# Kernel optimization log

Measured on AMD Instinct MI355X. Metric: run time of the kernel, lower is better.

Reference implementation:

```python
import jax, jax.numpy as jnp
import numpy as np

N = 50000          # n_sample
F = 64             # n_feature
DEG = 16           # edges per node
E = N * DEG
HID = 256          # n_hidden
NCLS = 16          # n_class
NPOOL = 3
K = 2              # propagation steps
ALPHA = 1.0        # Propagation alpha
EPS = 1e-5
NODE_POOL = round(N ** (1.0 / NPOOL))          # 37
N0 = round(N / NODE_POOL)                      # 1351
N1 = round(N0 / NODE_POOL)                     # 37
N2 = round(N1 / NODE_POOL)                     # 1


def setup_inputs():
    key = jax.random.key(0)
    ks = jax.random.split(key, 16)
    x = jax.random.normal(ks[0], (N, F), jnp.float32)
    x_cov = jax.random.uniform(ks[1], (N, F), jnp.float32)
    adj_rows = jnp.asarray(np.repeat(np.arange(N, dtype=np.int32), DEG))  # sorted
    adj_cols = jax.random.randint(ks[2], (E,), 0, N, jnp.int32)
    adj_vals = jax.random.uniform(ks[3], (E,), jnp.float32)
    feature_corr = jax.random.uniform(ks[4], (N2, F), jnp.float32)
    bn_gamma = jnp.ones((F,), jnp.float32)
    bn_beta = jnp.zeros((F,), jnp.float32)
    lin = lambda k, i, o: jax.random.normal(k, (i, o), jnp.float32) * 0.05
    W0 = lin(ks[5], F, HID); C0 = jax.random.normal(ks[6], (N0, HID), jnp.float32) * 0.05
    W1 = lin(ks[7], F, HID); C1 = jax.random.normal(ks[8], (N1, HID), jnp.float32) * 0.05
    W2 = lin(ks[9], F, HID); C2 = jax.random.normal(ks[10], (N2, HID), jnp.float32) * 0.05
    mW1 = lin(ks[11], 2 * F, HID); mb1 = jnp.zeros((HID,), jnp.float32)
    mp1 = jnp.full((1,), 0.25, jnp.float32)
    mW2 = lin(ks[12], HID, HID); mb2 = jnp.zeros((HID,), jnp.float32)
    mp2 = jnp.full((1,), 0.25, jnp.float32)
    mW3 = lin(ks[13], HID, NCLS); mb3 = jnp.zeros((NCLS,), jnp.float32)
    return dict(x=x, x_cov=x_cov, adj_vals=adj_vals, feature_corr=feature_corr,
                bn_gamma=bn_gamma, bn_beta=bn_beta, W0=W0, C0=C0, W1=W1, C1=C1,
                W2=W2, C2=C2, mW1=mW1, mb1=mb1, mp1=mp1, mW2=mW2, mb2=mb2, mp2=mp2,
                mW3=mW3, mb3=mb3, adj_rows=adj_rows, adj_cols=adj_cols)


def _pool(xc, W, C, nc):
    # ClusteringLayer: project, hard-assign to nearest centroid, mean-pool,
    # corr = per-node squared deviation from its cluster mean (input resolution).
    h = xc @ W                                                    # [n_prev, HID]
    d = (h * h).sum(-1, keepdims=True) - 2.0 * (h @ C.T) + (C * C).sum(-1)[None, :]
    a = jnp.argmin(d, axis=1)                                     # [n_prev] cluster ids
    cnt = jax.ops.segment_sum(jnp.ones((xc.shape[0],), xc.dtype), a, num_segments=nc)
    pooled = jax.ops.segment_sum(xc, a, num_segments=nc) / jnp.maximum(cnt, 1.0)[:, None]
    corr = (xc - pooled[a]) ** 2                                  # [n_prev, F]
    return pooled, corr, a


def _forward(x, x_cov, adj_vals, feature_corr, bn_gamma, bn_beta, W0, C0, W1, C1,
             W2, C2, mW1, mb1, mp1, mW2, mb2, mp2, mW3, mb3, adj_rows, adj_cols):
    # BatchNorm1d (batch statistics)
    mu = x.mean(0)
    var = x.var(0)
    x = (x - mu) / jnp.sqrt(var + EPS) * bn_gamma + bn_beta
    x0 = x
    # pooling hierarchy
    p0, corr0, a0 = _pool(x_cov, W0, C0, N0)
    p1, corr1, a1 = _pool(p0, W1, C1, N1)
    p2, corr2, a2 = _pool(p1, W2, C2, N2)
    loss = (corr1.mean(0) + corr2.mean(0)).mean() / (NPOOL - 1)
    # gains: spmm(hard assignment, corr_next) is a gather
    g0 = 2.0 * jax.nn.sigmoid(corr2[a1] - corr1)          # [N0, F]
    g1 = 2.0 * jax.nn.sigmoid(feature_corr[a2] - corr2)   # [N1, F]
    # composed node->level cluster ids (masks[1] = masks[0] @ masks[1])
    cl0 = a0               # [N]
    cl1 = a1[a0]           # [N]
    r, c = adj_rows, adj_cols
    # (M diag(g) M^T)[r,c] = g[cl(r)]^2 * 1[cl(r)==cl(c)], masked to adj pattern
    same0 = (cl0[r] == cl0[c])[:, None]
    same1 = (cl1[r] == cl1[c])[:, None]
    vals = adj_vals[:, None] \
        + jnp.where(same0, (g0 * g0)[cl0[r]], jnp.float32(0)) \
        + jnp.where(same1, (g1 * g1)[cl1[r]], jnp.float32(0))     # [E, F]
    # per-feature sparse row softmax
    m = jax.ops.segment_max(vals, r, num_segments=N)
    ev = jnp.exp(vals - m[r])
    s = jax.ops.segment_sum(ev, r, num_segments=N)
    A = ev / s[r]                                                  # [E, F]
    # k propagation steps: per-feature spmm + alpha * x0 residual
    for _ in range(K):
        x = jax.ops.segment_sum(A * x[c], r, num_segments=N) + ALPHA * x0
    # MLP head with PReLU, log-probabilities
    h = jnp.concatenate([x, x0], axis=1)
    h = h @ mW1 + mb1
    h = jnp.where(h >= 0, h, mp1 * h)
    h = h @ mW2 + mb2
    h = jnp.where(h >= 0, h, mp2 * h)
    logits = h @ mW3 + mb3
    out = jax.nn.log_softmax(logits, axis=1)
    return out, loss


def reference(x, x_cov, adj_vals, feature_corr, bn_gamma, bn_beta, W0, C0, W1, C1,
              W2, C2, mW1, mb1, mp1, mW2, mb2, mp2, mW3, mb3, adj_rows, adj_cols):
    return _forward(x, x_cov, adj_vals, feature_corr, bn_gamma, bn_beta, W0, C0,
                    W1, C1, W2, C2, mW1, mb1, mp1, mW2, mb2, mp2, mW3, mb3,
                    adj_rows, adj_cols)
```

## Files before the change

kernel.cpp:

```cpp
#include <hip/hip_runtime.h>
#include <math.h>

#define N_NODES 50000
#define FEA 64
#define DEG 16
#define HID 256
#define NCLS 16
#define NP0 1351
#define NP0T 1408
#define CTILES 11
#define NP1 37
#define EPSV 1e-5f

__global__ __launch_bounds__(256) void bn_reduce(const float* __restrict__ x,
                                                 float* __restrict__ bnsum, float* __restrict__ bnsq) {
    __shared__ float s1[256], s2[256];
    int tid = threadIdx.x;
    int f = tid & 63, sub = tid >> 6;
    float a = 0.f, b = 0.f;
    for (int r = blockIdx.x * 4 + sub; r < N_NODES; r += gridDim.x * 4) {
        float v = x[r * FEA + f];
        a += v; b += v * v;
    }
    s1[tid] = a; s2[tid] = b;
    __syncthreads();
    if (tid < 64) {
        a = s1[tid] + s1[tid + 64] + s1[tid + 128] + s1[tid + 192];
        b = s2[tid] + s2[tid + 64] + s2[tid + 128] + s2[tid + 192];
        atomicAdd(&bnsum[tid], a);
        atomicAdd(&bnsq[tid], b);
    }
}

__global__ __launch_bounds__(256) void bn_apply(const float* __restrict__ x,
                                                const float* __restrict__ bnsum, const float* __restrict__ bnsq,
                                                const float* __restrict__ gamma, const float* __restrict__ beta,
                                                float* __restrict__ x0) {
    int gid = blockIdx.x * 256 + threadIdx.x;
    if (gid >= N_NODES * FEA) return;
    int f = gid & 63;
    float mu = bnsum[f] * (1.0f / N_NODES);
    float var = bnsq[f] * (1.0f / N_NODES) - mu * mu;
    float sc = gamma[f] / sqrtf(var + EPSV);
    x0[gid] = (x[gid] - mu) * sc + beta[f];
}

__global__ void transpose_W0(const float* __restrict__ W0, float* __restrict__ W0t) {
    int idx = blockIdx.x * 256 + threadIdx.x;
    if (idx < FEA * HID) {
        int f = idx >> 8, h = idx & 255;
        W0t[h * FEA + f] = W0[idx];
    }
}

__global__ __launch_bounds__(64) void compute_G2(const float* __restrict__ W0t, const float* __restrict__ C0,
                                                 float* __restrict__ Gt, float* __restrict__ c0n) {
    int j = blockIdx.x, k = threadIdx.x;
    if (j >= NP0) {
        Gt[k * NP0T + j] = 0.f;
        if (k == 0) c0n[j] = 3.4e38f;
        return;
    }
    const float* c = C0 + j * HID;
    float acc = 0.f;
    for (int m = 0; m < HID; ++m) acc += W0t[m * FEA + k] * c[m];
    Gt[k * NP0T + j] = acc;
    float cn = 0.f;
    for (int m = k; m < HID; m += 64) { float v = c[m]; cn += v * v; }
    for (int off = 32; off; off >>= 1) cn += __shfl_xor(cn, off);
    if (k == 0) c0n[j] = cn;
}

__global__ void cnorm(const float* __restrict__ C, float* __restrict__ cn) {
    int j = blockIdx.x, k = threadIdx.x;
    const float* c = C + j * HID;
    float acc = 0.f;
    for (int m = k; m < HID; m += 64) { float v = c[m]; acc += v * v; }
    for (int off = 32; off; off >>= 1) acc += __shfl_xor(acc, off);
    if (k == 0) cn[j] = acc;
}

__global__ __launch_bounds__(256, 3) void argmin0_split(const float* __restrict__ xcov,
                                                        const float* __restrict__ Gt,
                                                        const float* __restrict__ c0n,
                                                        unsigned long long* __restrict__ amin) {
    __shared__ float As[64 * 140];
    __shared__ float Bs[32 * 128];
    __shared__ float cs[128];
    int t = threadIdx.x;
    int row0 = (blockIdx.x >> 2) * 128;
    int chunk = blockIdx.x & 3;
    int tile0 = chunk * 3;
    int tile1 = tile0 + 3; if (tile1 > CTILES) tile1 = CTILES;

    {
        int r = t & 127, half = t >> 7;
        int row = row0 + r;
        int fr = r + 4 * (r >> 5);
        if (row < N_NODES) {
            const float4* xp = (const float4*)(xcov + (size_t)row * FEA + half * 32);
            #pragma unroll
            for (int u = 0; u < 8; ++u) {
                float4 v = xp[u];
                int k = half * 32 + u * 4;
                As[(k+0)*140 + fr] = v.x; As[(k+1)*140 + fr] = v.y;
                As[(k+2)*140 + fr] = v.z; As[(k+3)*140 + fr] = v.w;
            }
        } else {
            #pragma unroll
            for (int u = 0; u < 8; ++u) {
                int k = half * 32 + u * 4;
                As[(k+0)*140+fr] = 0.f; As[(k+1)*140+fr] = 0.f;
                As[(k+2)*140+fr] = 0.f; As[(k+3)*140+fr] = 0.f;
            }
        }
    }

    int tr = t & 15, tc = t >> 4;
    int aoff = 8 * tr + 4 * (tr >> 2);
    int boff = 8 * tc;
    int bkk = t >> 3, bpart = t & 7;
    unsigned long long best[8];
    #pragma unroll
    for (int r = 0; r < 8; ++r) best[r] = ~0ull;

    for (int tile = tile0; tile < tile1; ++tile) {
        int j0 = tile * 128;
        float acc[8][8];
        #pragma unroll
        for (int r = 0; r < 8; ++r)
            #pragma unroll
            for (int c = 0; c < 8; ++c) acc[r][c] = 0.f;

        for (int kh = 0; kh < 2; ++kh) {
            __syncthreads();
            {
                const float* gr = Gt + (size_t)(kh * 32 + bkk) * NP0T + j0;
                #pragma unroll
                for (int u = 0; u < 4; ++u) {
                    int gi = bpart + 8 * u;
                    float4 v = *(const float4*)(gr + gi * 4);
                    *(float4*)(Bs + bkk * 128 + gi * 4) = v;
                }
            }
            if (kh == 0 && t < 128) cs[t] = c0n[j0 + t];
            __syncthreads();
            #pragma unroll 4
            for (int k2 = 0; k2 < 32; ++k2) {
                int k = kh * 32 + k2;
                float4 av0 = *(const float4*)(As + k * 140 + aoff);
                float4 av1 = *(const float4*)(As + k * 140 + aoff + 4);
                float4 bv0 = *(const float4*)(Bs + k2 * 128 + boff);
                float4 bv1 = *(const float4*)(Bs + k2 * 128 + boff + 4);
                float av[8] = {av0.x, av0.y, av0.z, av0.w, av1.x, av1.y, av1.z, av1.w};
                float bv[8] = {bv0.x, bv0.y, bv0.z, bv0.w, bv1.x, bv1.y, bv1.z, bv1.w};
                #pragma unroll
                for (int r = 0; r < 8; ++r)
                    #pragma unroll
                    for (int c = 0; c < 8; ++c) acc[r][c] += av[r] * bv[c];
            }
        }
        #pragma unroll
        for (int c = 0; c < 8; ++c) {
            int j = j0 + boff + c;
            float cn = cs[boff + c];
            #pragma unroll
            for (int r = 0; r < 8; ++r) {
                float d = cn - 2.0f * acc[r][c];
                unsigned s = __float_as_uint(d);
                unsigned u2 = ((int)s < 0) ? ~s : (s | 0x80000000u);
                unsigned long long p = ((unsigned long long)u2 << 32) | (unsigned)j;
                if (p < best[r]) best[r] = p;
            }
        }
    }

    __syncthreads();
    unsigned long long* pmin = (unsigned long long*)Bs;
    #pragma unroll
    for (int r = 0; r < 8; ++r) pmin[(8 * tr + r) * 16 + tc] = best[r];
    __syncthreads();
    if (t < 128) {
        unsigned long long b = pmin[t * 16];
        #pragma unroll
        for (int q = 1; q < 16; ++q) {
            unsigned long long v = pmin[t * 16 + q];
            if (v < b) b = v;
        }
        int row = row0 + t;
        if (row < N_NODES) atomicMin(&amin[row], b);
    }
}

__global__ __launch_bounds__(256) void hist0(const unsigned long long* __restrict__ amin,
                                             int* __restrict__ a0, int* __restrict__ hist) {
    int i = blockIdx.x * 256 + threadIdx.x;
    bool act = i < N_NODES;
    int j = act ? (int)(unsigned)amin[i] : -1;
    if (act) a0[i] = j;
    unsigned long long todo = __ballot(act);
    int lane = threadIdx.x & 63;
    while (todo) {
        int leader = __ffsll((long long)todo) - 1;
        int lj = __shfl(j, leader);
        unsigned long long grp = __ballot(act && j == lj);
        if (lane == leader) atomicAdd(&hist[lj], __popcll(grp));
        todo &= ~grp;
    }
}

__global__ __launch_bounds__(256) void scan0(const int* __restrict__ hist, int* __restrict__ off,
                                             int* __restrict__ cursor) {
    __shared__ int wsum[4];
    int t = threadIdx.x;
    int c0 = t * 6;
    int loc[6]; int s = 0;
    #pragma unroll
    for (int u = 0; u < 6; ++u) {
        int j = c0 + u;
        int h = (j < NP0) ? hist[j] : 0;
        loc[u] = s; s += h;
    }
    int lane = t & 63, w = t >> 6;
    int v = s;
    #pragma unroll
    for (int d = 1; d < 64; d <<= 1) {
        int up = __shfl_up(v, d);
        if (lane >= d) v += up;
    }
    if (lane == 63) wsum[w] = v;
    __syncthreads();
    int woff = 0;
    for (int q = 0; q < w; ++q) woff += wsum[q];
    int excl = woff + v - s;
    #pragma unroll
    for (int u = 0; u < 6; ++u) {
        int j = c0 + u;
        if (j < NP0) { off[j] = excl + loc[u]; cursor[j] = excl + loc[u]; }
    }
    if (t == 255) off[NP0] = excl + s;
}

__global__ __launch_bounds__(256) void scatter0(const int* __restrict__ a0, int* __restrict__ cursor,
                                                int* __restrict__ order, int* __restrict__ csrt) {
    int i = blockIdx.x * 256 + threadIdx.x;
    bool act = i < N_NODES;
    int j = act ? a0[i] : -1;
    int lane = threadIdx.x & 63;
    unsigned long long todo = __ballot(act);
    int pos = 0;
    while (todo) {
        int leader = __ffsll((long long)todo) - 1;
        int lj = __shfl(j, leader);
        unsigned long long grp = __ballot(act && j == lj);
        int base = 0;
        if (lane == leader) base = atomicAdd(&cursor[lj], __popcll(grp));
        base = __shfl(base, leader);
        if (act && j == lj)
            pos = base + __popcll(grp & ((1ull << lane) - 1ull));
        todo &= ~grp;
    }
    if (act) { order[pos] = i; csrt[pos] = j; }
}

__global__ __launch_bounds__(256) void pool0seg(const int* __restrict__ order, const int* __restrict__ csrt,
                                                const float* __restrict__ xcov, double* __restrict__ p0d) {
    int lane = threadIdx.x & 63;
    int w = threadIdx.x >> 6;
    int base = (blockIdx.x * 4 + w) * 16;
    if (base >= N_NODES) return;
    int n = N_NODES - base; if (n > 16) n = 16;
    float vals[16]; int cl[16];
    #pragma unroll
    for (int r = 0; r < 16; ++r) {
        if (r < n) {
            int idx = order[base + r];
            cl[r] = csrt[base + r];
            vals[r] = xcov[(size_t)idx * FEA + lane];
        } else { cl[r] = -1; vals[r] = 0.f; }
    }
    double acc = (double)vals[0]; int cur = cl[0];
    #pragma unroll
    for (int r = 1; r < 16; ++r) {
        if (r < n) {
            if (cl[r] == cur) { acc += (double)vals[r]; }
            else { atomicAdd(&p0d[(size_t)cur * FEA + lane], acc); acc = (double)vals[r]; cur = cl[r]; }
        }
    }
    atomicAdd(&p0d[(size_t)cur * FEA + lane], acc);
}

__global__ void pool_fin0(const double* __restrict__ p0d, const int* __restrict__ hist,
                          float* __restrict__ p0, int total) {
    int gid = blockIdx.x * 256 + threadIdx.x;
    if (gid < total) p0[gid] = (float)(p0d[gid] / (double)max(hist[gid >> 6], 1));
}

__global__ __launch_bounds__(64) void level1(const float* __restrict__ p0, const float* __restrict__ W1,
                                             const float* __restrict__ C1, const float* __restrict__ c1n,
                                             int* __restrict__ a1) {
    int i = blockIdx.x;
    int lane = threadIdx.x;
    const float* pr = p0 + (size_t)i * FEA;
    float h[4] = {0.f, 0.f, 0.f, 0.f};
    for (int k = 0; k < FEA; ++k) {
        float pv = pr[k];
        #pragma unroll
        for (int q = 0; q < 4; ++q) h[q] += pv * W1[k * HID + q * 64 + lane];
    }
    float hh = h[0]*h[0] + h[1]*h[1] + h[2]*h[2] + h[3]*h[3];
    for (int off = 32; off; off >>= 1) hh += __shfl_xor(hh, off);
    float best = 3.4e38f; int bj = 0;
    for (int j = 0; j < NP1; ++j) {
        const float* cj = C1 + j * HID;
        float dp = h[0]*cj[lane] + h[1]*cj[64+lane] + h[2]*cj[128+lane] + h[3]*cj[192+lane];
        for (int off = 32; off; off >>= 1) dp += __shfl_xor(dp, off);
        float d = hh - 2.0f * dp + c1n[j];
        if (d < best) { best = d; bj = j; }
    }
    if (lane == 0) a1[i] = bj;
}

#define P1W 16
__global__ __launch_bounds__(1024) void pool1(const float* __restrict__ p0, const int* __restrict__ a1,
                                              float* __restrict__ p1) {
    __shared__ int a1s[NP0];
    __shared__ int lists[NP0 + P1W];
    __shared__ float psum[P1W][64];
    __shared__ int pcnt[P1W];
    int j = blockIdx.x;
    int t = threadIdx.x;
    int lane = t & 63, w = t >> 6;
    for (int i = t; i < NP0; i += 1024) a1s[i] = a1[i];
    __syncthreads();
    const int per = (NP0 + P1W - 1) / P1W;
    int s0 = w * per;
    int s1 = s0 + per; if (s1 > NP0) s1 = NP0;
    int cnt = 0;
    for (int base = s0; base < s1; base += 64) {
        int i = base + lane;
        bool m = (i < s1) && (a1s[i] == j);
        unsigned long long mask = __ballot(m);
        int rank = __popcll(mask & ((1ull << lane) - 1ull));
        if (m) lists[s0 + cnt + rank] = i;
        cnt += __popcll(mask);
    }
    float acc = 0.f;
    int m4 = cnt & ~3;
    for (int m = 0; m < m4; m += 4) {
        int i0 = lists[s0 + m], i1 = lists[s0 + m + 1], i2 = lists[s0 + m + 2], i3 = lists[s0 + m + 3];
        float v0 = p0[i0 * FEA + lane];
        float v1 = p0[i1 * FEA + lane];
        float v2 = p0[i2 * FEA + lane];
        float v3 = p0[i3 * FEA + lane];
        acc += ((v0 + v1) + (v2 + v3));
    }
    for (int m = m4; m < cnt; ++m) acc += p0[lists[s0 + m] * FEA + lane];
    psum[w][lane] = acc;
    if (lane == 0) pcnt[w] = cnt;
    __syncthreads();
    if (w == 0) {
        float s = 0.f; int c = 0;
        #pragma unroll
        for (int q = 0; q < P1W; ++q) { s += psum[q][lane]; c += pcnt[q]; }
        p1[j * FEA + lane] = s / fmaxf((float)c, 1.0f);
    }
}

__global__ __launch_bounds__(256) void level2(const float* __restrict__ p1, const float* __restrict__ fc,
                                              float* __restrict__ corr2, float* __restrict__ g1sq,
                                              float* __restrict__ loss2f) {
    __shared__ float p2s[64];
    __shared__ float lacc[64];
    int tid = threadIdx.x;
    if (tid < 64) {
        float s = 0.f;
        for (int i = 0; i < NP1; ++i) s += p1[i * FEA + tid];
        p2s[tid] = s * (1.0f / NP1);
        lacc[tid] = 0.f;
    }
    __syncthreads();
    for (int t = tid; t < NP1 * FEA; t += 256) {
        int f = t & 63;
        float dv = p1[t] - p2s[f];
        float c2 = dv * dv;
        corr2[t] = c2;
        float sg = 2.0f / (1.0f + __expf(-(fc[f] - c2)));
        g1sq[t] = sg * sg;
        atomicAdd(&lacc[f], c2);
    }
    __syncthreads();
    if (tid < 64) loss2f[tid] = lacc[tid] * (1.0f / NP1);
}

__global__ __launch_bounds__(256) void corr1_g0(const float* __restrict__ p0, const float* __restrict__ p1,
                                                const int* __restrict__ a1, const float* __restrict__ corr2,
                                                float* __restrict__ g0sq, float* __restrict__ loss1g) {
    __shared__ float sh[256];
    int tid = threadIdx.x;
    int f = tid & 63, sub = tid >> 6;
    int i = blockIdx.x * 4 + sub;
    float c1v = 0.f;
    if (i < NP0) {
        int a = a1[i];
        float dv = p0[i * FEA + f] - p1[a * FEA + f];
        c1v = dv * dv;
        float sg = 2.0f / (1.0f + __expf(-(corr2[a * FEA + f] - c1v)));
        g0sq[i * FEA + f] = sg * sg;
    }
    sh[tid] = c1v;
    __syncthreads();
    if (tid < 64) atomicAdd(&loss1g[tid], sh[tid] + sh[tid+64] + sh[tid+128] + sh[tid+192]);
}

__global__ void loss_final(const float* __restrict__ loss1g, const float* __restrict__ loss2f,
                           float* __restrict__ out_loss) {
    int lane = threadIdx.x;
    float v = loss1g[lane] * (1.0f / NP0) + loss2f[lane];
    for (int off = 32; off; off >>= 1) v += __shfl_xor(v, off);
    if (lane == 0) out_loss[0] = v * (1.0f / FEA) * 0.5f;
}

__global__ void cl1map(const int* __restrict__ a0, const int* __restrict__ a1, int* __restrict__ cl1) {
    int i = blockIdx.x * 256 + threadIdx.x;
    if (i < N_NODES) cl1[i] = a1[a0[i]];
}

__global__ __launch_bounds__(256) void prop(const float* __restrict__ xin, const float* __restrict__ x0,
                                            const int* __restrict__ cols, const float* __restrict__ avals,
                                            const int* __restrict__ cl0, const int* __restrict__ cl1,
                                            const float* __restrict__ g0sq, const float* __restrict__ g1sq,
                                            float* __restrict__ xout) {
    int lane = threadIdx.x & 63;
    int i = blockIdx.x * 4 + __builtin_amdgcn_readfirstlane(threadIdx.x >> 6);
    int s0 = cl0[i], s1 = cl1[i];
    float g0f = g0sq[s0 * FEA + lane];
    float g1f = g1sq[s1 * FEA + lane];
    float x0f = x0[(size_t)i * FEA + lane];
    int ce[DEG]; float v[DEG];
    float m = -3.4e38f;
    #pragma unroll
    for (int e = 0; e < DEG; ++e) {
        int c = cols[i * DEG + e];
        ce[e] = c;
        float val = avals[i * DEG + e];
        if (cl0[c] == s0) val += g0f;
        if (cl1[c] == s1) val += g1f;
        v[e] = val;
        m = fmaxf(m, val);
    }
    float se = 0.f, acc = 0.f;
    #pragma unroll
    for (int e = 0; e < DEG; ++e) {
        float w = __expf(v[e] - m);
        se += w;
        acc += w * xin[(size_t)ce[e] * FEA + lane];
    }
    xout[(size_t)i * FEA + lane] = acc / se + x0f;
}

__global__ __launch_bounds__(256, 3) void gemm_prelu(const float* __restrict__ s0, const float* __restrict__ s1,
                                                     const float* __restrict__ s2, const float* __restrict__ s3,
                                                     int nchunks, int lda,
                                                     const float* __restrict__ W, const float* __restrict__ b,
                                                     const float* __restrict__ pp, float* __restrict__ out) {
    __shared__ float As[64 * 140];
    __shared__ float Bs[32 * 128];
    int t = threadIdx.x;
    int mt = blockIdx.x >> 1, nt = blockIdx.x & 1;
    int row0 = mt * 128, n0 = nt * 128;
    int tr = t & 15, tc = t >> 4;
    int aoff = 8 * tr + 4 * (tr >> 2);
    int boff = 8 * tc;

    float acc[8][8];
    #pragma unroll
    for (int r = 0; r < 8; ++r)
        #pragma unroll
        for (int c = 0; c < 8; ++c) acc[r][c] = 0.f;

    int ar = t & 127, ahalf = t >> 7;
    int arow = row0 + ar;
    int afr = ar + 4 * (ar >> 5);
    int bkk = t >> 3, bpart = t & 7;

    for (int c = 0; c < nchunks; ++c) {
        const float* Ap = (c == 0) ? s0 : (c == 1) ? s1 : (c == 2) ? s2 : s3;
        __syncthreads();
        if (arow < N_NODES) {
            const float4* xp = (const float4*)(Ap + (size_t)arow * lda + ahalf * 32);
            #pragma unroll
            for (int u = 0; u < 8; ++u) {
                float4 v = xp[u];
                int k = ahalf * 32 + u * 4;
                As[(k+0)*140 + afr] = v.x; As[(k+1)*140 + afr] = v.y;
                As[(k+2)*140 + afr] = v.z; As[(k+3)*140 + afr] = v.w;
            }
        } else {
            #pragma unroll
            for (int u = 0; u < 8; ++u) {
                int k = ahalf * 32 + u * 4;
                As[(k+0)*140+afr] = 0.f; As[(k+1)*140+afr] = 0.f;
                As[(k+2)*140+afr] = 0.f; As[(k+3)*140+afr] = 0.f;
            }
        }
        for (int kh = 0; kh < 2; ++kh) {
            __syncthreads();
            {
                const float* wr = W + (size_t)(c * 64 + kh * 32 + bkk) * HID + n0;
                #pragma unroll
                for (int u = 0; u < 4; ++u) {
                    int ci = (bpart + 8 * u) * 4;
                    float4 v = *(const float4*)(wr + ci);
                    *(float4*)(Bs + bkk * 128 + ci) = v;
                }
            }
            __syncthreads();
            #pragma unroll 4
            for (int k2 = 0; k2 < 32; ++k2) {
                int k = kh * 32 + k2;
                float4 av0 = *(const float4*)(As + k * 140 + aoff);
                float4 av1 = *(const float4*)(As + k * 140 + aoff + 4);
                float4 bv0 = *(const float4*)(Bs + k2 * 128 + boff);
                float4 bv1 = *(const float4*)(Bs + k2 * 128 + boff + 4);
                float av[8] = {av0.x, av0.y, av0.z, av0.w, av1.x, av1.y, av1.z, av1.w};
                float bv[8] = {bv0.x, bv0.y, bv0.z, bv0.w, bv1.x, bv1.y, bv1.z, bv1.w};
                #pragma unroll
                for (int r = 0; r < 8; ++r)
                    #pragma unroll
                    for (int cc = 0; cc < 8; ++cc) acc[r][cc] += av[r] * bv[cc];
            }
        }
    }
    float p = pp[0];
    float bb[8];
    #pragma unroll
    for (int cc = 0; cc < 8; ++cc) bb[cc] = b[n0 + 8 * tc + cc];
    #pragma unroll
    for (int r = 0; r < 8; ++r) {
        int row = row0 + 8 * tr + r;
        if (row >= N_NODES) break;
        float* o = out + (size_t)row * HID + n0 + 8 * tc;
        float4 o0, o1;
        float h;
        h = acc[r][0] + bb[0]; o0.x = h >= 0.f ? h : p * h;
        h = acc[r][1] + bb[1]; o0.y = h >= 0.f ? h : p * h;
        h = acc[r][2] + bb[2]; o0.z = h >= 0.f ? h : p * h;
        h = acc[r][3] + bb[3]; o0.w = h >= 0.f ? h : p * h;
        h = acc[r][4] + bb[4]; o1.x = h >= 0.f ? h : p * h;
        h = acc[r][5] + bb[5]; o1.y = h >= 0.f ? h : p * h;
        h = acc[r][6] + bb[6]; o1.z = h >= 0.f ? h : p * h;
        h = acc[r][7] + bb[7]; o1.w = h >= 0.f ? h : p * h;
        *(float4*)(o) = o0;
        *(float4*)(o + 4) = o1;
    }
}

__global__ __launch_bounds__(256) void mlp3(const float* __restrict__ hin, const float* __restrict__ W3,
                                            const float* __restrict__ b3, float* __restrict__ out) {
    __shared__ float Ws[HID * NCLS];
    int tid = threadIdx.x;
    for (int t = tid; t < HID * NCLS; t += 256) Ws[t] = W3[t];
    __syncthreads();
    int lane = tid & 63;
    int wv = __builtin_amdgcn_readfirstlane(tid >> 6);
    int rs = lane >> 4, c = lane & 15;
    int row = blockIdx.x * 16 + wv * 4 + rs;
    const float4* hr = (const float4*)(hin + (size_t)row * HID);
    float acc = b3[c];
    for (int k4 = 0; k4 < 64; ++k4) {
        float4 h = hr[k4];
        int k = k4 * 4;
        acc += h.x * Ws[k * NCLS + c];
        acc += h.y * Ws[(k + 1) * NCLS + c];
        acc += h.z * Ws[(k + 2) * NCLS + c];
        acc += h.w * Ws[(k + 3) * NCLS + c];
    }
    float m = acc;
    #pragma unroll
    for (int off = 1; off < 16; off <<= 1) m = fmaxf(m, __shfl_xor(m, off));
    float e = __expf(acc - m);
    float s = e;
    #pragma unroll
    for (int off = 1; off < 16; off <<= 1) s += __shfl_xor(s, off);
    out[(size_t)row * NCLS + c] = acc - m - __logf(s);
}

extern "C" void kernel_launch(void* const* d_in, const int* in_sizes, int n_in,
                              void* d_out, int out_size, void* d_ws, size_t ws_size,
                              hipStream_t stream) {
    const float* x     = (const float*)d_in[0];
    const float* xcov  = (const float*)d_in[1];
    const float* avals = (const float*)d_in[2];
    const float* fc    = (const float*)d_in[3];
    const float* gamma = (const float*)d_in[4];
    const float* beta  = (const float*)d_in[5];
    const float* W0    = (const float*)d_in[6];
    const float* C0    = (const float*)d_in[7];
    const float* W1    = (const float*)d_in[8];
    const float* C1    = (const float*)d_in[9];
    const float* mW1   = (const float*)d_in[12];
    const float* mb1   = (const float*)d_in[13];
    const float* mp1   = (const float*)d_in[14];
    const float* mW2   = (const float*)d_in[15];
    const float* mb2   = (const float*)d_in[16];
    const float* mp2   = (const float*)d_in[17];
    const float* mW3   = (const float*)d_in[18];
    const float* mb3   = (const float*)d_in[19];
    const int* cols    = (const int*)d_in[21];

    float* ws = (float*)d_ws;
    size_t off = 0;
    auto alloc = [&](size_t n) { float* p = ws + off; off += (n + 63) & ~(size_t)63; return p; };

    float* x0    = alloc((size_t)N_NODES * FEA);
    float* h1b   = alloc((size_t)N_NODES * HID);
    float* h2b   = alloc((size_t)N_NODES * HID);
    float* W0t   = alloc(HID * FEA);
    float* Gt    = alloc((size_t)FEA * NP0T);
    float* c0n   = alloc(NP0T);
    float* c1n   = alloc(NP1);
    float* g0sq  = alloc(NP0 * FEA);
    float* g1sq  = alloc(NP1 * FEA);
    float* corr2 = alloc(NP1 * FEA);
    float* loss2f= alloc(64);
    float* p1    = alloc(NP1 * FEA);
    float* p0    = alloc(NP0 * FEA);
    int*   a0    = (int*)alloc(N_NODES);
    int*   cl1   = (int*)alloc(N_NODES);
    int*   a1    = (int*)alloc(NP0);
    int*   order = (int*)alloc(N_NODES);
    int*   csrt  = (int*)alloc(N_NODES);
    int*   offj  = (int*)alloc(NP0 + 1);
    int*   cursor= (int*)alloc(NP0);
    unsigned long long* amin = (unsigned long long*)alloc((size_t)N_NODES * 2);
    float* zero0 = ws + off;
    float* bnsum = alloc(64);
    float* bnsq  = alloc(64);
    int*   hist  = (int*)alloc(NP0);
    float* loss1g= alloc(64);
    double* p0d  = (double*)alloc((size_t)NP0 * FEA * 2);
    size_t zbytes = (size_t)((ws + off) - zero0) * sizeof(float);

    float* xb1 = h1b;
    float* xb2 = h2b;
    float* outp = (float*)d_out;

    hipMemsetAsync(zero0, 0, zbytes, stream);
    hipMemsetAsync(amin, 0xFF, (size_t)N_NODES * 8, stream);

    bn_reduce<<<256, 256, 0, stream>>>(x, bnsum, bnsq);
    bn_apply<<<(N_NODES * FEA) / 256, 256, 0, stream>>>(x, bnsum, bnsq, gamma, beta, x0);

    transpose_W0<<<(FEA * HID + 255) / 256, 256, 0, stream>>>(W0, W0t);
    compute_G2<<<NP0T, 64, 0, stream>>>(W0t, C0, Gt, c0n);
    cnorm<<<NP1, 64, 0, stream>>>(C1, c1n);

    int mtiles = (N_NODES + 127) / 128;
    argmin0_split<<<mtiles * 4, 256, 0, stream>>>(xcov, Gt, c0n, amin);

    hist0<<<(N_NODES + 255) / 256, 256, 0, stream>>>(amin, a0, hist);
    scan0<<<1, 256, 0, stream>>>(hist, offj, cursor);
    scatter0<<<(N_NODES + 255) / 256, 256, 0, stream>>>(a0, cursor, order, csrt);
    pool0seg<<<(N_NODES + 63) / 64, 256, 0, stream>>>(order, csrt, xcov, p0d);
    pool_fin0<<<(NP0 * FEA + 255) / 256, 256, 0, stream>>>(p0d, hist, p0, NP0 * FEA);

    level1<<<NP0, 64, 0, stream>>>(p0, W1, C1, c1n, a1);
    pool1<<<NP1, 1024, 0, stream>>>(p0, a1, p1);

    level2<<<1, 256, 0, stream>>>(p1, fc, corr2, g1sq, loss2f);
    corr1_g0<<<(NP0 + 3) / 4, 256, 0, stream>>>(p0, p1, a1, corr2, g0sq, loss1g);
    loss_final<<<1, 64, 0, stream>>>(loss1g, loss2f, outp + (size_t)N_NODES * NCLS);

    cl1map<<<(N_NODES + 255) / 256, 256, 0, stream>>>(a0, a1, cl1);

    prop<<<N_NODES / 4, 256, 0, stream>>>(x0, x0, cols, avals, a0, cl1, g0sq, g1sq, xb1);
    prop<<<N_NODES / 4, 256, 0, stream>>>(xb1, x0, cols, avals, a0, cl1, g0sq, g1sq, xb2);

    int gemmGrid = mtiles * 2;
    gemm_prelu<<<gemmGrid, 256, 0, stream>>>(xb2, x0, nullptr, nullptr, 2, FEA,
                                             mW1, mb1, mp1, h1b);
    gemm_prelu<<<gemmGrid, 256, 0, stream>>>(h1b, h1b + 64, h1b + 128, h1b + 192, 4, HID,
                                             mW2, mb2, mp2, h2b);
    mlp3<<<N_NODES / 16, 256, 0, stream>>>(h2b, mW3, mb3, outp);
}
```

Baseline: 707.1 us.

## Load GEMM B operand straight from global into registers, drop shared B tiles

```diff
diff --git a/kernel.cpp b/kernel.cpp
--- a/kernel.cpp
+++ b/kernel.cpp
@@ -80,13 +80,11 @@
     if (k == 0) cn[j] = acc;
 }
 
-__global__ __launch_bounds__(256, 3) void argmin0_split(const float* __restrict__ xcov,
-                                                        const float* __restrict__ Gt,
-                                                        const float* __restrict__ c0n,
-                                                        unsigned long long* __restrict__ amin) {
+__global__ __launch_bounds__(256, 4) void argmin0_breg(const float* __restrict__ xcov,
+                                                       const float* __restrict__ Gt,
+                                                       const float* __restrict__ c0n,
+                                                       unsigned long long* __restrict__ amin) {
     __shared__ float As[64 * 140];
-    __shared__ float Bs[32 * 128];
-    __shared__ float cs[128];
     int t = threadIdx.x;
     int row0 = (blockIdx.x >> 2) * 128;
     int chunk = blockIdx.x & 3;
@@ -115,11 +113,11 @@
             }
         }
     }
+    __syncthreads();
 
     int tr = t & 15, tc = t >> 4;
     int aoff = 8 * tr + 4 * (tr >> 2);
     int boff = 8 * tc;
-    int bkk = t >> 3, bpart = t & 7;
     unsigned long long best[8];
     #pragma unroll
     for (int r = 0; r < 8; ++r) best[r] = ~0ull;
@@ -132,41 +130,33 @@
             #pragma unroll
             for (int c = 0; c < 8; ++c) acc[r][c] = 0.f;
 
-        for (int kh = 0; kh < 2; ++kh) {
-            __syncthreads();
-            {
-                const float* gr = Gt + (size_t)(kh * 32 + bkk) * NP0T + j0;
+        const float* bp = Gt + j0 + boff;
+        float4 bv0 = *(const float4*)(bp);
+        float4 bv1 = *(const float4*)(bp + 4);
+        for (int k = 0; k < 64; ++k) {
+            float4 av0 = *(const float4*)(As + k * 140 + aoff);
+            float4 av1 = *(const float4*)(As + k * 140 + aoff + 4);
+            float4 cb0 = bv0, cb1 = bv1;
+            int kn = (k < 63) ? k + 1 : 63;
+            const float* np = Gt + (size_t)kn * NP0T + j0 + boff;
+            bv0 = *(const float4*)(np);
+            bv1 = *(const float4*)(np + 4);
+            float av[8] = {av0.x, av0.y, av0.z, av0.w, av1.x, av1.y, av1.z, av1.w};
+            float bv[8] = {cb0.x, cb0.y, cb0.z, cb0.w, cb1.x, cb1.y, cb1.z, cb1.w};
+            #pragma unroll
+            for (int r = 0; r < 8; ++r)
                 #pragma unroll
-                for (int u = 0; u < 4; ++u) {
-                    int gi = bpart + 8 * u;
-                    float4 v = *(const float4*)(gr + gi * 4);
-                    *(float4*)(Bs + bkk * 128 + gi * 4) = v;
-                }
-            }
-            if (kh == 0 && t < 128) cs[t] = c0n[j0 + t];
-            __syncthreads();
-            #pragma unroll 4
-            for (int k2 = 0; k2 < 32; ++k2) {
-                int k = kh * 32 + k2;
-                float4 av0 = *(const float4*)(As + k * 140 + aoff);
-                float4 av1 = *(const float4*)(As + k * 140 + aoff + 4);
-                float4 bv0 = *(const float4*)(Bs + k2 * 128 + boff);
-                float4 bv1 = *(const float4*)(Bs + k2 * 128 + boff + 4);
-                float av[8] = {av0.x, av0.y, av0.z, av0.w, av1.x, av1.y, av1.z, av1.w};
-                float bv[8] = {bv0.x, bv0.y, bv0.z, bv0.w, bv1.x, bv1.y, bv1.z, bv1.w};
-                #pragma unroll
-                for (int r = 0; r < 8; ++r)
-                    #pragma unroll
-                    for (int c = 0; c < 8; ++c) acc[r][c] += av[r] * bv[c];
-            }
-        }
+                for (int c = 0; c < 8; ++c) acc[r][c] += av[r] * bv[c];
+        }
+        float4 cn0 = *(const float4*)(c0n + j0 + boff);
+        float4 cn1 = *(const float4*)(c0n + j0 + boff + 4);
+        float cn[8] = {cn0.x, cn0.y, cn0.z, cn0.w, cn1.x, cn1.y, cn1.z, cn1.w};
         #pragma unroll
         for (int c = 0; c < 8; ++c) {
             int j = j0 + boff + c;
-            float cn = cs[boff + c];
             #pragma unroll
             for (int r = 0; r < 8; ++r) {
-                float d = cn - 2.0f * acc[r][c];
+                float d = cn[c] - 2.0f * acc[r][c];
                 unsigned s = __float_as_uint(d);
                 unsigned u2 = ((int)s < 0) ? ~s : (s | 0x80000000u);
                 unsigned long long p = ((unsigned long long)u2 << 32) | (unsigned)j;
@@ -176,7 +166,7 @@
     }
 
     __syncthreads();
-    unsigned long long* pmin = (unsigned long long*)Bs;
+    unsigned long long* pmin = (unsigned long long*)As;
     #pragma unroll
     for (int r = 0; r < 8; ++r) pmin[(8 * tr + r) * 16 + tc] = best[r];
     __syncthreads();
@@ -465,7 +455,6 @@
                                                      const float* __restrict__ W, const float* __restrict__ b,
                                                      const float* __restrict__ pp, float* __restrict__ out) {
     __shared__ float As[64 * 140];
-    __shared__ float Bs[32 * 128];
     int t = threadIdx.x;
     int mt = blockIdx.x >> 1, nt = blockIdx.x & 1;
     int row0 = mt * 128, n0 = nt * 128;
@@ -482,65 +471,65 @@
     int ar = t & 127, ahalf = t >> 7;
     int arow = row0 + ar;
     int afr = ar + 4 * (ar >> 5);
-    int bkk = t >> 3, bpart = t & 7;
+
+    float4 areg[8];
+    {
+        if (arow < N_NODES) {
+            const float4* xp = (const float4*)(s0 + (size_t)arow * lda + ahalf * 32);
+            #pragma unroll
+            for (int u = 0; u < 8; ++u) areg[u] = xp[u];
+        } else {
+            #pragma unroll
+            for (int u = 0; u < 8; ++u) areg[u] = make_float4(0.f, 0.f, 0.f, 0.f);
+        }
+    }
 
     for (int c = 0; c < nchunks; ++c) {
-        const float* Ap = (c == 0) ? s0 : (c == 1) ? s1 : (c == 2) ? s2 : s3;
         __syncthreads();
-        if (arow < N_NODES) {
-            const float4* xp = (const float4*)(Ap + (size_t)arow * lda + ahalf * 32);
-            #pragma unroll
-            for (int u = 0; u < 8; ++u) {
-                float4 v = xp[u];
-                int k = ahalf * 32 + u * 4;
-                As[(k+0)*140 + afr] = v.x; As[(k+1)*140 + afr] = v.y;
-                As[(k+2)*140 + afr] = v.z; As[(k+3)*140 + afr] = v.w;
+        #pragma unroll
+        for (int u = 0; u < 8; ++u) {
+            int k = ahalf * 32 + u * 4;
+            As[(k+0)*140 + afr] = areg[u].x; As[(k+1)*140 + afr] = areg[u].y;
+            As[(k+2)*140 + afr] = areg[u].z; As[(k+3)*140 + afr] = areg[u].w;
+        }
+        if (c + 1 < nchunks) {
+            const float* An = (c + 1 == 1) ? s1 : (c + 1 == 2) ? s2 : s3;
+            if (arow < N_NODES) {
+                const float4* xp = (const float4*)(An + (size_t)arow * lda + ahalf * 32);
+                #pragma unroll
+                for (int u = 0; u < 8; ++u) areg[u] = xp[u];
             }
-        } else {
-            #pragma unroll
-            for (int u = 0; u < 8; ++u) {
-                int k = ahalf * 32 + u * 4;
-                As[(k+0)*140+afr] = 0.f; As[(k+1)*140+afr] = 0.f;
-                As[(k+2)*140+afr] = 0.f; As[(k+3)*140+afr] = 0.f;
-            }
-        }
-        for (int kh = 0; kh < 2; ++kh) {
-            __syncthreads();
-            {
-                const float* wr = W + (size_t)(c * 64 + kh * 32 + bkk) * HID + n0;
+        }
+        __syncthreads();
+
+        const float* wbase = W + (size_t)(c * 64) * HID + n0 + boff;
+        float4 bv0 = *(const float4*)(wbase);
+        float4 bv1 = *(const float4*)(wbase + 4);
+        for (int k = 0; k < 64; ++k) {
+            float4 av0 = *(const float4*)(As + k * 140 + aoff);
+            float4 av1 = *(const float4*)(As + k * 140 + aoff + 4);
+            float4 cb0 = bv0, cb1 = bv1;
+            int kn = (k < 63) ? k + 1 : 63;
+            const float* np = wbase + (size_t)kn * HID;
+            bv0 = *(const float4*)(np);
+            bv1 = *(const float4*)(np + 4);
+            float av[8] = {av0.x, av0.y, av0.z, av0.w, av1.x, av1.y, av1.z, av1.w};
+            float bv[8] = {cb0.x, cb0.y, cb0.z, cb0.w, cb1.x, cb1.y, cb1.z, cb1.w};
+            #pragma unroll
+            for (int r = 0; r < 8; ++r)
                 #pragma unroll
-                for (int u = 0; u < 4; ++u) {
-                    int ci = (bpart + 8 * u) * 4;
-                    float4 v = *(const float4*)(wr + ci);
-                    *(float4*)(Bs + bkk * 128 + ci) = v;
-                }
-            }
-            __syncthreads();
-            #pragma unroll 4
-            for (int k2 = 0; k2 < 32; ++k2) {
-                int k = kh * 32 + k2;
-                float4 av0 = *(const float4*)(As + k * 140 + aoff);
-                float4 av1 = *(const float4*)(As + k * 140 + aoff + 4);
-                float4 bv0 = *(const float4*)(Bs + k2 * 128 + boff);
-                float4 bv1 = *(const float4*)(Bs + k2 * 128 + boff + 4);
-                float av[8] = {av0.x, av0.y, av0.z, av0.w, av1.x, av1.y, av1.z, av1.w};
-                float bv[8] = {bv0.x, bv0.y, bv0.z, bv0.w, bv1.x, bv1.y, bv1.z, bv1.w};
-                #pragma unroll
-                for (int r = 0; r < 8; ++r)
-                    #pragma unroll
-                    for (int cc = 0; cc < 8; ++cc) acc[r][cc] += av[r] * bv[cc];
-            }
+                for (int cc = 0; cc < 8; ++cc) acc[r][cc] += av[r] * bv[cc];
         }
     }
     float p = pp[0];
     float bb[8];
     #pragma unroll
-    for (int cc = 0; cc < 8; ++cc) bb[cc] = b[n0 + 8 * tc + cc];
+    for (int cc = 0; cc < 8; ++cc) bb[cc] = b[n0 + boff + cc];
     #pragma unroll
     for (int r = 0; r < 8; ++r) {
         int row = row0 + 8 * tr + r;
         if (row >= N_NODES) break;
-        float* o = out + (size_t)row * HID + n0 + 8 * tc;
+        float* o = out + (size_t)row * HID + n0 + boff;
         float4 o0, o1;
         float h;
         h = acc[r][0] + bb[0]; o0.x = h >= 0.f ? h : p * h;
@@ -657,7 +646,7 @@
     cnorm<<<NP1, 64, 0, stream>>>(C1, c1n);
 
     int mtiles = (N_NODES + 127) / 128;
-    argmin0_split<<<mtiles * 4, 256, 0, stream>>>(xcov, Gt, c0n, amin);
+    argmin0_breg<<<mtiles * 4, 256, 0, stream>>>(xcov, Gt, c0n, amin);
 
     hist0<<<(N_NODES + 255) / 256, 256, 0, stream>>>(amin, a0, hist);
     scan0<<<1, 256, 0, stream>>>(hist, offj, cursor);
```

After: 1.293 ms. 1.83x slower.
